# Kernel tuning notes

Hardware: AMD Instinct MI355X
Metric: run time of the kernel (lower is better)

The kernel has to match this reference:

```python
import jax, jax.numpy as jnp
import numpy as np

B, S, H, DFF, HD = 2, 8192, 1024, 4096, 128


def setup_inputs() -> dict:
    key = jax.random.key(0)
    ks = jax.random.split(key, 10)
    hidden_states = jax.random.normal(ks[0], (B, S, H), jnp.float32)
    labels = jax.random.randint(ks[1], (B, S), 0, 32000)
    labels = jnp.where(jax.random.uniform(ks[2], (B, S)) < 0.1, -100, labels).astype(jnp.int64)
    cos = jax.random.normal(ks[3], (B, S, HD), jnp.float32)
    sin = jax.random.normal(ks[4], (B, S, HD), jnp.float32)
    cu_seq_lens_q = (jnp.arange(B + 1) * S).astype(jnp.int32)
    # gate params: random (instead of the degenerate all-keep init) so the mask varies
    Wg = jax.random.normal(ks[5], (H, 1), jnp.float32) * 0.05
    bg = jnp.zeros((1,), jnp.float32)
    # wrapped layer instantiated as a token-wise FFN: relu(x W1 + b1) W2 + b2
    W1 = jax.random.normal(ks[6], (H, DFF), jnp.float32) * 0.02
    b1 = jnp.zeros((DFF,), jnp.float32)
    W2 = jax.random.normal(ks[7], (DFF, H), jnp.float32) * 0.02
    b2 = jnp.zeros((H,), jnp.float32)
    return {"hidden_states": hidden_states, "cos": cos, "sin": sin,
            "Wg": Wg, "bg": bg, "W1": W1, "b1": b1, "W2": W2, "b2": b2,
            "labels": labels, "cu_seq_lens_q": cu_seq_lens_q}


def reference(hidden_states, cos, sin, Wg, bg, W1, b1, W2, b2, labels, cu_seq_lens_q):
    # per-token gate in fp32: sigmoid(Linear(h -> 1))
    logits = hidden_states.astype(jnp.float32) @ Wg + bg          # [B,S,1]
    w = jax.nn.sigmoid(logits).astype(hidden_states.dtype)         # [B,S,1]
    # keep mask: gate >= 0.5, force-keep ignored-label tokens
    mask = (w[..., 0] >= 0.5) | (labels == -100)                   # [B,S]
    # scale kept tokens by the gate weight before the wrapped layer
    xg = hidden_states * w                                         # [B,S,H]
    # token-wise wrapped layer (FFN): gather->layer->scatter == mask * layer(xg)
    y = jax.nn.relu(xg @ W1 + b1) @ W2 + b2                        # [B,S,H]
    # dropped tokens produce exact zeros in the output (scatter into zeros_like)
    out = jnp.where(mask[..., None], y, jnp.zeros_like(y))
    return out
```

## Files before the change

kernel.cpp:

```cpp
#include <hip/hip_runtime.h>
#include <hip/hip_bf16.h>


#define TOK 16384
#define HID 1024
#define FF  4096

typedef __attribute__((ext_vector_type(8))) __bf16 bf16x8;
typedef __attribute__((ext_vector_type(4))) float f32x4;

__device__ __forceinline__ void gload_lds16(const void* g, void* l) {
  __builtin_amdgcn_global_load_lds((const __attribute__((address_space(1))) void*)g,
                                   (__attribute__((address_space(3))) void*)l, 16, 0, 0);
}

#define GTOK 16
#define NBT1 1024
#define NBT2 1024

__global__ __launch_bounds__(256) void k_pre(const float* __restrict__ W1,
                                             __hip_bfloat16* __restrict__ W1t,
                                             const float* __restrict__ W2,
                                             __hip_bfloat16* __restrict__ W2t,
                                             const float* __restrict__ h,
                                             const float* __restrict__ wg,
                                             const float* __restrict__ bgp,
                                             const int* __restrict__ labels,
                                             float* __restrict__ out,
                                             __hip_bfloat16* __restrict__ A,
                                             int* __restrict__ idx,
                                             int* __restrict__ cnt) {
  const int bid = blockIdx.x;
  const int tid = threadIdx.x;

  if (bid < NBT1 + NBT2) {
    const float* src;
    __hip_bfloat16* dst;
    int R, C, tb;
    if (bid < NBT1) { src = W1; dst = W1t; R = HID; C = FF;  tb = bid; }
    else            { src = W2; dst = W2t; R = FF;  C = HID; tb = bid - NBT1; }
    const int nbc = C / 64;
    const int c0 = (tb % nbc) * 64, r0 = (tb / nbc) * 64;
    __shared__ float tile[64][65];
    const int tx = tid & 63, ty = tid >> 6;
#pragma unroll
    for (int i = 0; i < 16; ++i)
      tile[ty + i * 4][tx] = src[(size_t)(r0 + ty + i * 4) * C + (c0 + tx)];
    __syncthreads();
#pragma unroll
    for (int i = 0; i < 16; ++i)
      dst[(size_t)(c0 + ty + i * 4) * R + (r0 + tx)] =
          __float2bfloat16(tile[tx][ty + i * 4]);
    return;
  }

  const int gb = bid - (NBT1 + NBT2);
  const int t0 = gb * GTOK;
  const int wave = tid >> 6, lane = tid & 63;

  float4 gv[4];
#pragma unroll
  for (int it = 0; it < 4; ++it) gv[it] = ((const float4*)wg)[it * 64 + lane];

  float4 hv[4][4];
  __shared__ float slogit[GTOK];
  __shared__ int sslot[GTOK];

#pragma unroll
  for (int r = 0; r < 4; ++r) {
    const int li = r * 4 + wave;
    const float* hrow = h + (size_t)(t0 + li) * HID;
    float d = 0.f;
#pragma unroll
    for (int it = 0; it < 4; ++it) {
      hv[r][it] = ((const float4*)hrow)[it * 64 + lane];
      d += hv[r][it].x * gv[it].x + hv[r][it].y * gv[it].y +
           hv[r][it].z * gv[it].z + hv[r][it].w * gv[it].w;
    }
#pragma unroll
    for (int o = 32; o > 0; o >>= 1) d += __shfl_down(d, o, 64);
    if (lane == 0) slogit[li] = d;
  }
  __syncthreads();

  if (tid == 0) {
    const float bg = bgp[0];
    int slots[GTOK];
    int n = 0;
#pragma unroll
    for (int li = 0; li < GTOK; ++li) {
      const bool keep = (slogit[li] + bg >= 0.0f) || (labels[t0 + li] == -100);
      slots[li] = keep ? n++ : -1;
    }
    const int base = atomicAdd(cnt, n);
#pragma unroll
    for (int li = 0; li < GTOK; ++li)
      sslot[li] = slots[li] >= 0 ? base + slots[li] : -1;
  }
  __syncthreads();

#pragma unroll
  for (int r = 0; r < 4; ++r) {
    const int li = r * 4 + wave;
    const int t = t0 + li;
    const int m = sslot[li];
    if (m >= 0) {
      if (lane == 0) idx[m] = t;
      const float logit = slogit[li] + bgp[0];
      const float w = 1.0f / (1.0f + __expf(-logit));
#pragma unroll
      for (int it = 0; it < 4; ++it) {
        union { ushort4 u; __hip_bfloat16 b[4]; } pk;
        pk.b[0] = __float2bfloat16(hv[r][it].x * w);
        pk.b[1] = __float2bfloat16(hv[r][it].y * w);
        pk.b[2] = __float2bfloat16(hv[r][it].z * w);
        pk.b[3] = __float2bfloat16(hv[r][it].w * w);
        ((ushort4*)(A + (size_t)m * HID))[it * 64 + lane] = pk.u;
      }
    } else {
      const float4 z = make_float4(0.f, 0.f, 0.f, 0.f);
#pragma unroll
      for (int it = 0; it < 4; ++it)
        ((float4*)(out + (size_t)t * HID))[it * 64 + lane] = z;
    }
  }
}


__global__ __launch_bounds__(256, 2) void k_gemm1(const __hip_bfloat16* __restrict__ A,
                                                  const __hip_bfloat16* __restrict__ Bt,
                                                  const float* __restrict__ bias,
                                                  __hip_bfloat16* __restrict__ Act,
                                                  const int* __restrict__ cnt) {
  const int Mc = *cnt;
  const int m0 = blockIdx.x * 128;
  if (m0 >= Mc) return;
  const int n0 = blockIdx.y * 128;

  __shared__ __hip_bfloat16 lA[128 * 64];
  __shared__ __hip_bfloat16 lB[128 * 64];

  const int tid = threadIdx.x;
  const int wave = tid >> 6, lane = tid & 63;
  const int wr = (wave >> 1) * 64, wc = (wave & 1) * 64;
  const int fm = lane & 15, quad = lane >> 4;

  const int srow = (lane >> 3);
  const int sg   = ((lane & 7) ^ srow) * 8;

  f32x4 acc[4][4] = {};

  const __hip_bfloat16* gA = A  + (size_t)(m0 + wave * 32 + srow) * HID + sg;
  const __hip_bfloat16* gB = Bt + (size_t)(n0 + wave * 32 + srow) * HID + sg;
  char* dA = (char*)lA + wave * 4096;
  char* dB = (char*)lB + wave * 4096;

  for (int kt = 0; kt < HID; kt += 64) {
    __syncthreads();
#pragma unroll
    for (int c = 0; c < 4; ++c) {
      gload_lds16(gA + (size_t)(c * 8) * HID + kt, dA + c * 1024);
      gload_lds16(gB + (size_t)(c * 8) * HID + kt, dB + c * 1024);
    }
    __syncthreads();
#pragma unroll
    for (int ks = 0; ks < 2; ++ks) {
      bf16x8 af[4], bb[4];
#pragma unroll
      for (int i = 0; i < 4; ++i)
        af[i] = *(const bf16x8*)&lA[(wr + i * 16 + fm) * 64 + (((ks * 4 + quad) ^ (fm & 7)) * 8)];
#pragma unroll
      for (int j = 0; j < 4; ++j)
        bb[j] = *(const bf16x8*)&lB[(wc + j * 16 + fm) * 64 + (((ks * 4 + quad) ^ (fm & 7)) * 8)];
#pragma unroll
      for (int i = 0; i < 4; ++i)
#pragma unroll
        for (int j = 0; j < 4; ++j)
          acc[i][j] = __builtin_amdgcn_mfma_f32_16x16x32_bf16(af[i], bb[j], acc[i][j], 0, 0, 0);
    }
  }

#pragma unroll
  for (int j = 0; j < 4; ++j) {
    const int col = n0 + wc + j * 16 + fm;
    const float bv = bias[col];
#pragma unroll
    for (int i = 0; i < 4; ++i) {
      const int rbase = m0 + wr + i * 16 + quad * 4;
#pragma unroll
      for (int r = 0; r < 4; ++r) {
        float v = acc[i][j][r] + bv;
        v = v > 0.f ? v : 0.f;
        Act[(size_t)(rbase + r) * FF + col] = __float2bfloat16(v);
      }
    }
  }
}

__global__ __launch_bounds__(256, 4) void k_gemm2(const __hip_bfloat16* __restrict__ Act,
                                                  const __hip_bfloat16* __restrict__ Bt,
                                                  const float* __restrict__ bias,
                                                  const int* __restrict__ idx,
                                                  float* __restrict__ out,
                                                  const int* __restrict__ cnt) {
  const int Mc = *cnt;
  const int m0 = blockIdx.x * 64;
  if (m0 >= Mc) return;
  const int n0 = blockIdx.y * 128;

  __shared__ __hip_bfloat16 lA[64 * 64];
  __shared__ __hip_bfloat16 lB[128 * 64];

  const int tid = threadIdx.x;
  const int wave = tid >> 6, lane = tid & 63;
  const int wr = (wave >> 1) * 32, wc = (wave & 1) * 64;
  const int fm = lane & 15, quad = lane >> 4;
  const int srow = (lane >> 3);
  const int sg   = ((lane & 7) ^ srow) * 8;

  f32x4 acc[2][4] = {};

  const __hip_bfloat16* gA = Act + (size_t)(m0 + wave * 16 + srow) * FF + sg;
  const __hip_bfloat16* gB = Bt  + (size_t)(n0 + wave * 32 + srow) * FF + sg;
  char* dA = (char*)lA + wave * 2048;
  char* dB = (char*)lB + wave * 4096;

  for (int kt = 0; kt < FF; kt += 64) {
    __syncthreads();
#pragma unroll
    for (int c = 0; c < 2; ++c)
      gload_lds16(gA + (size_t)(c * 8) * FF + kt, dA + c * 1024);
#pragma unroll
    for (int c = 0; c < 4; ++c)
      gload_lds16(gB + (size_t)(c * 8) * FF + kt, dB + c * 1024);
    __syncthreads();
#pragma unroll
    for (int ks = 0; ks < 2; ++ks) {
      bf16x8 af[2], bb[4];
#pragma unroll
      for (int i = 0; i < 2; ++i)
        af[i] = *(const bf16x8*)&lA[(wr + i * 16 + fm) * 64 + (((ks * 4 + quad) ^ (fm & 7)) * 8)];
#pragma unroll
      for (int j = 0; j < 4; ++j)
        bb[j] = *(const bf16x8*)&lB[(wc + j * 16 + fm) * 64 + (((ks * 4 + quad) ^ (fm & 7)) * 8)];
#pragma unroll
      for (int i = 0; i < 2; ++i)
#pragma unroll
        for (int j = 0; j < 4; ++j)
          acc[i][j] = __builtin_amdgcn_mfma_f32_16x16x32_bf16(af[i], bb[j], acc[i][j], 0, 0, 0);
    }
  }

#pragma unroll
  for (int i = 0; i < 2; ++i) {
#pragma unroll
    for (int r = 0; r < 4; ++r) {
      const int m = m0 + wr + i * 16 + quad * 4 + r;
      if (m < Mc) {
        const int t = idx[m];
        float* orow = out + (size_t)t * HID + n0 + wc + fm;
#pragma unroll
        for (int j = 0; j < 4; ++j)
          orow[j * 16] = acc[i][j][r] + bias[n0 + wc + j * 16 + fm];
      }
    }
  }
}

extern "C" void kernel_launch(void* const* d_in, const int* in_sizes, int n_in,
                              void* d_out, int out_size, void* d_ws, size_t ws_size,
                              hipStream_t stream) {
  const float* h   = (const float*)d_in[0];
  const float* Wg  = (const float*)d_in[3];
  const float* bg  = (const float*)d_in[4];
  const float* W1  = (const float*)d_in[5];
  const float* b1  = (const float*)d_in[6];
  const float* W2  = (const float*)d_in[7];
  const float* b2  = (const float*)d_in[8];
  const int*  labels = (const int*)d_in[9];
  float* out = (float*)d_out;

  char* ws = (char*)d_ws;
  int* cnt            = (int*)(ws + 0);
  int* idx            = (int*)(ws + 1024);
  __hip_bfloat16* W1t = (__hip_bfloat16*)(ws + (1u  << 17));
  __hip_bfloat16* W2t = (__hip_bfloat16*)(ws + (16u << 20));
  __hip_bfloat16* A   = (__hip_bfloat16*)(ws + (32u << 20));
  __hip_bfloat16* Act = (__hip_bfloat16*)(ws + (64ull << 20));

  hipMemsetAsync(cnt, 0, 4, stream);
  k_pre<<<NBT1 + NBT2 + TOK / GTOK, 256, 0, stream>>>(W1, W1t, W2, W2t, h, Wg,
                                                      bg, labels, out, A, idx, cnt);
  k_gemm1<<<dim3(TOK / 128, FF / 128), 256, 0, stream>>>(A, W1t, b1, Act, cnt);
  k_gemm2<<<dim3(TOK / 64, HID / 128), 256, 0, stream>>>(Act, W2t, b2, idx, out, cnt);
}
```

Measured before the change: 368.2 us.

## Double-buffer LDS tiles in second GEMM with async prefetch overlap

The second FFN GEMM now keeps two LDS buffers per operand. It issues the global-to-LDS loads for the next K tile before computing on the current one, and uses explicit vmcnt waits and raw barriers in place of __syncthreads. The aim is to hide global load latency behind the MFMA work. In exchange the LDS footprint doubles and the occupancy hint drops from 4 to 3 blocks per CU.

```diff
diff --git a/kernel.cpp b/kernel.cpp
--- a/kernel.cpp
+++ b/kernel.cpp
@@ -8,6 +8,10 @@
 
 typedef __attribute__((ext_vector_type(8))) __bf16 bf16x8;
 typedef __attribute__((ext_vector_type(4))) float f32x4;
+
+#define VMW(n) asm volatile("s_waitcnt vmcnt(" #n ")" ::: "memory")
+#define LKW0() asm volatile("s_waitcnt lgkmcnt(0)" ::: "memory")
+#define CFENCE() asm volatile("" ::: "memory")
 
 __device__ __forceinline__ void gload_lds16(const void* g, void* l) {
   __builtin_amdgcn_global_load_lds((const __attribute__((address_space(1))) void*)g,
@@ -197,7 +201,7 @@
   }
 }
 
-__global__ __launch_bounds__(256, 4) void k_gemm2(const __hip_bfloat16* __restrict__ Act,
+__global__ __launch_bounds__(256, 3) void k_gemm2(const __hip_bfloat16* __restrict__ Act,
                                                   const __hip_bfloat16* __restrict__ Bt,
                                                   const float* __restrict__ bias,
                                                   const int* __restrict__ idx,
@@ -208,8 +212,8 @@
   if (m0 >= Mc) return;
   const int n0 = blockIdx.y * 128;
 
-  __shared__ __hip_bfloat16 lA[64 * 64];
-  __shared__ __hip_bfloat16 lB[128 * 64];
+  __shared__ __hip_bfloat16 lA[2][64 * 64];
+  __shared__ __hip_bfloat16 lB[2][128 * 64];
 
   const int tid = threadIdx.x;
   const int wave = tid >> 6, lane = tid & 63;
@@ -222,33 +226,44 @@
 
   const __hip_bfloat16* gA = Act + (size_t)(m0 + wave * 16 + srow) * FF + sg;
   const __hip_bfloat16* gB = Bt  + (size_t)(n0 + wave * 32 + srow) * FF + sg;
-  char* dA = (char*)lA + wave * 2048;
-  char* dB = (char*)lB + wave * 4096;
-
-  for (int kt = 0; kt < FF; kt += 64) {
-    __syncthreads();
+
+  auto stage = [&](int b, int kt) {
+    char* dA = (char*)lA[b] + wave * 2048;
+    char* dB = (char*)lB[b] + wave * 4096;
 #pragma unroll
     for (int c = 0; c < 2; ++c)
       gload_lds16(gA + (size_t)(c * 8) * FF + kt, dA + c * 1024);
 #pragma unroll
     for (int c = 0; c < 4; ++c)
       gload_lds16(gB + (size_t)(c * 8) * FF + kt, dB + c * 1024);
-    __syncthreads();
+  };
+
+  stage(0, 0);
+  const int NT = FF / 64;
+  for (int t = 0; t < NT; ++t) {
+    const int cur = t & 1;
+    if (t + 1 < NT) { stage(cur ^ 1, (t + 1) * 64); VMW(6); }
+    else            { VMW(0); }
+    __builtin_amdgcn_s_barrier(); CFENCE();
+    const __hip_bfloat16* sA = lA[cur];
+    const __hip_bfloat16* sB = lB[cur];
 #pragma unroll
     for (int ks = 0; ks < 2; ++ks) {
       bf16x8 af[2], bb[4];
 #pragma unroll
       for (int i = 0; i < 2; ++i)
-        af[i] = *(const bf16x8*)&lA[(wr + i * 16 + fm) * 64 + (((ks * 4 + quad) ^ (fm & 7)) * 8)];
+        af[i] = *(const bf16x8*)&sA[(wr + i * 16 + fm) * 64 + (((ks * 4 + quad) ^ (fm & 7)) * 8)];
 #pragma unroll
       for (int j = 0; j < 4; ++j)
-        bb[j] = *(const bf16x8*)&lB[(wc + j * 16 + fm) * 64 + (((ks * 4 + quad) ^ (fm & 7)) * 8)];
+        bb[j] = *(const bf16x8*)&sB[(wc + j * 16 + fm) * 64 + (((ks * 4 + quad) ^ (fm & 7)) * 8)];
 #pragma unroll
       for (int i = 0; i < 2; ++i)
 #pragma unroll
         for (int j = 0; j < 4; ++j)
           acc[i][j] = __builtin_amdgcn_mfma_f32_16x16x32_bf16(af[i], bb[j], acc[i][j], 0, 0, 0);
     }
+    LKW0();
+    __builtin_amdgcn_s_barrier(); CFENCE();
   }
 
 #pragma unroll
```

New measurement: 372.8 us. Within noise of the previous version (+1.2%).
